# Optimization experiments

Measured on AMD Instinct MI355X. Metric: run time of the kernel, lower is better.

The kernel has to match this reference:

```python
import jax, jax.numpy as jnp
import numpy as np
from jax import lax

# --- static config (matches init_kwargs) ---
K_NAT, P_NAT, NHEAD, DM, L = 5, 2, 8, 128, 3
PK, OV, STRIDE = 4, 2, 2          # patcher kernel / overlap / stride = PK-OV
PPAD = PK - OV                    # circular pad for patcher/depatcher crop
RK, RC = 5, 12                    # res layer kernel, hidden channels = 3*4
DN = ('NCHW', 'OIHW', 'NCHW')


def setup_inputs() -> dict:
    key = jax.random.key(0)
    ks = jax.random.split(key, 16)
    B, C, H, W = 2, 3, 256, 256
    rn = lambda k, shape, s=0.02: jax.random.normal(k, shape, jnp.float32) * s
    return {
        'x': jax.random.normal(ks[0], (B, C, H, W), jnp.float32),
        'pos_w': jax.random.uniform(ks[1], (C, H, W), jnp.float32) + 0.5,
        'pos_b': jax.random.uniform(ks[2], (C, H, W), jnp.float32) - 0.5,
        'patch_w': rn(ks[3], (DM, C, PK, PK), 0.05),
        'patch_b': jnp.zeros((DM,), jnp.float32),
        'ln1_g': jnp.ones((L, DM), jnp.float32),
        'ln1_b': jnp.zeros((L, DM), jnp.float32),
        'qkv_w': rn(ks[4], (L, 3 * DM, DM)),
        'qkv_b': jnp.zeros((L, 3 * DM), jnp.float32),
        'rpb': rn(ks[5], (L, NHEAD, 2 * K_NAT - 1, 2 * K_NAT - 1)),
        'proj_w': rn(ks[6], (L, DM, DM)),
        'proj_b': jnp.zeros((L, DM), jnp.float32),
        'ln2_g': jnp.ones((L, DM), jnp.float32),
        'ln2_b': jnp.zeros((L, DM), jnp.float32),
        'fc1_w': rn(ks[7], (L, 4 * DM, DM)),
        'fc1_b': jnp.zeros((L, 4 * DM), jnp.float32),
        'fc2_w': rn(ks[8], (L, DM, 4 * DM)),
        'fc2_b': jnp.zeros((L, DM), jnp.float32),
        'depatch_w': rn(ks[9], (DM, C, PK, PK), 0.05),   # ConvTranspose2d weight (Cin,Cout,kh,kw)
        'depatch_b': jnp.zeros((C,), jnp.float32),
        'res_cv1_w': rn(ks[10], (RC, C, RK, RK), 0.05),
        'res_cv1_b': jnp.zeros((RC,), jnp.float32),
        'res_cv2_w': rn(ks[11], (C, RC, 1, 1), 0.05),
        'res_cv2_b': jnp.zeros((C,), jnp.float32),
    }


def _layer_norm(x, g, b):
    m = x.mean(-1, keepdims=True)
    v = x.var(-1, keepdims=True)
    return (x - m) * lax.rsqrt(v + 1e-5) * g + b


def _nat_block(x, ln1_g, ln1_b, qkv_w, qkv_b, rpb, proj_w, proj_b,
               ln2_g, ln2_b, fc1_w, fc1_b, fc2_w, fc2_b):
    # x: (B,H,W,C). NATLayer: LN -> circular pad by k//2 -> NA -> crop -> residual -> LN -> MLP -> residual.
    # After padding, every kept (interior) pixel has a full centered kxk neighborhood,
    # so we compute q only at interior positions and gather kxk K/V windows from the padded map.
    B, H, W, C = x.shape
    k, p, h = K_NAT, P_NAT, NHEAD
    dh = C // h
    y = _layer_norm(x, ln1_g, ln1_b)
    y = jnp.pad(y, ((0, 0), (p, p), (p, p), (0, 0)), mode='wrap')  # circular
    qkv = y @ qkv_w.T + qkv_b                                      # (B,H+2p,W+2p,3C)
    q, kk, vv = jnp.split(qkv, 3, axis=-1)
    q = q[:, p:p + H, p:p + W].reshape(B, H, W, h, dh) * (dh ** -0.5)
    def win(t):
        t = t.reshape(B, H + 2 * p, W + 2 * p, h, dh)
        return jnp.stack([t[:, i:i + H, j:j + W]
                          for i in range(k) for j in range(k)], axis=3)  # (B,H,W,k*k,h,dh)
    kw, vw = win(kk), win(vv)
    bias = rpb[:, p:p + k, p:p + k].reshape(h, k * k)  # centered slice of (2k-1,2k-1) RPB
    logits = jnp.einsum('bxyhd,bxynhd->bxyhn', q, kw) + bias
    a = jax.nn.softmax(logits, axis=-1)
    o = jnp.einsum('bxyhn,bxynhd->bxyhd', a, vw).reshape(B, H, W, C)
    x = x + (o @ proj_w.T + proj_b)
    y = _layer_norm(x, ln2_g, ln2_b)
    y = jax.nn.leaky_relu(y @ fc1_w.T + fc1_b) @ fc2_w.T + fc2_b
    return x + y


def _forward(x, pos_w, pos_b, patch_w, patch_b, ln1_g, ln1_b, qkv_w, qkv_b,
             rpb, proj_w, proj_b, ln2_g, ln2_b, fc1_w, fc1_b, fc2_w, fc2_b,
             depatch_w, depatch_b, res_cv1_w, res_cv1_b, res_cv2_w, res_cv2_b):
    # positional embedding (dropout is identity, p=0)
    x = x * pos_w + pos_b
    # OverlapConvPatcher: circular pad by (PK-OV), conv kernel PK stride PK-OV -> (B,129,129,DM)
    xp = jnp.pad(x, ((0, 0), (0, 0), (PPAD, PPAD), (PPAD, PPAD)), mode='wrap')
    f = lax.conv_general_dilated(xp, patch_w, (STRIDE, STRIDE), 'VALID',
                                 dimension_numbers=DN) + patch_b[None, :, None, None]
    f = f.transpose(0, 2, 3, 1)
    for i in range(L):
        f = _nat_block(f, ln1_g[i], ln1_b[i], qkv_w[i], qkv_b[i], rpb[i],
                       proj_w[i], proj_b[i], ln2_g[i], ln2_b[i],
                       fc1_w[i], fc1_b[i], fc2_w[i], fc2_b[i])
    # OverlapDeconvDepatcher: ConvTranspose2d (kernel PK, stride PK-OV), crop PPAD border
    f = f.transpose(0, 3, 1, 2)
    wf = jnp.flip(depatch_w, (2, 3)).transpose(1, 0, 2, 3)  # (Cout,Cin,kh,kw)
    y = lax.conv_general_dilated(f, wf, (1, 1), [(PK - 1, PK - 1)] * 2,
                                 lhs_dilation=(STRIDE, STRIDE),
                                 dimension_numbers=DN) + depatch_b[None, :, None, None]
    y = y[:, :, PPAD:-PPAD, PPAD:-PPAD]  # (B,3,256,256)
    # ResLayer: circular-pad same conv 5x5 -> leaky_relu -> 1x1 conv -> residual
    yp = jnp.pad(y, ((0, 0), (0, 0), (RK // 2, RK // 2), (RK // 2, RK // 2)), mode='wrap')
    r = lax.conv_general_dilated(yp, res_cv1_w, (1, 1), 'VALID',
                                 dimension_numbers=DN) + res_cv1_b[None, :, None, None]
    r = jax.nn.leaky_relu(r)
    r = lax.conv_general_dilated(r, res_cv2_w, (1, 1), 'VALID',
                                 dimension_numbers=DN) + res_cv2_b[None, :, None, None]
    return y + r


def reference(x, pos_w, pos_b, patch_w, patch_b, ln1_g, ln1_b, qkv_w, qkv_b,
              rpb, proj_w, proj_b, ln2_g, ln2_b, fc1_w, fc1_b, fc2_w, fc2_b,
              depatch_w, depatch_b, res_cv1_w, res_cv1_b, res_cv2_w, res_cv2_b):
    return _forward(x, pos_w, pos_b, patch_w, patch_b, ln1_g, ln1_b, qkv_w, qkv_b,
                    rpb, proj_w, proj_b, ln2_g, ln2_b, fc1_w, fc1_b, fc2_w, fc2_b,
                    depatch_w, depatch_b, res_cv1_w, res_cv1_b, res_cv2_w, res_cv2_b)
```

## Files before the change

### kernel.cpp

```cpp
#include <hip/hip_runtime.h>
#include <hip/hip_bf16.h>
#include <math.h>

#define HF 129
#define WF 129
#define BDIM 2
#define TOK (BDIM*HF*WF)
#define DMOD 128

typedef __attribute__((ext_vector_type(8))) short short8;
typedef __attribute__((ext_vector_type(8))) unsigned short ushort8;
typedef __attribute__((ext_vector_type(4))) float f32x4;

__device__ __forceinline__ float leaky(float v){ return v > 0.f ? v : 0.01f*v; }
__device__ __forceinline__ float bf2f(unsigned short u){ return __uint_as_float(((unsigned int)u) << 16); }
__device__ __forceinline__ unsigned short f2bf(float f){
    unsigned int u = __float_as_uint(f);
    unsigned int r = (u + 0x7fff + ((u >> 16) & 1)) >> 16;
    return (unsigned short)r;
}

#define NQ 147456
#define NPJ 49152
#define N1 196608
#define N2 196608
#define NPAT 8192
#define NDEP 8192
__global__ __launch_bounds__(256) void prep_weights(
    const float* __restrict__ qkv_w, const float* __restrict__ proj_w,
    const float* __restrict__ fc1_w, const float* __restrict__ fc2_w,
    const float* __restrict__ patch_w, const float* __restrict__ dep_w,
    __hip_bfloat16* __restrict__ wq, __hip_bfloat16* __restrict__ wp,
    __hip_bfloat16* __restrict__ w1, __hip_bfloat16* __restrict__ w2,
    __hip_bfloat16* __restrict__ wpat, __hip_bfloat16* __restrict__ wdep,
    float* __restrict__ zero64)
{
    int off = blockIdx.x*256 + threadIdx.x;
    if (off < NQ) { wq[off] = __float2bfloat16(qkv_w[off]); return; } off -= NQ;
    if (off < NPJ){ wp[off] = __float2bfloat16(proj_w[off]); return; } off -= NPJ;
    if (off < N1) { w1[off] = __float2bfloat16(fc1_w[off]); return; } off -= N1;
    if (off < N2) { w2[off] = __float2bfloat16(fc2_w[off]); return; } off -= N2;
    if (off < NPAT){ int r = off>>6, e = off&63;
        wpat[off] = __float2bfloat16(e < 48 ? patch_w[r*48 + e] : 0.f); return; } off -= NPAT;
    if (off < NDEP){ int e = off>>7, d = off&127;
        wdep[off] = __float2bfloat16(e < 48 ? dep_w[d*48 + e] : 0.f); return; } off -= NDEP;
    if (off < 64) zero64[off] = 0.f;
}

__global__ __launch_bounds__(256) void im2col_kernel(
    const float* __restrict__ x, const float* __restrict__ pos_w, const float* __restrict__ pos_b,
    __hip_bfloat16* __restrict__ G)
{
    __shared__ float xs[12][260];
    int blk = blockIdx.x;
    int b = blk / HF, oh = blk - b*HF;
    int tid = threadIdx.x;
    #pragma unroll
    for (int it = 0; it < 3; ++it) {
        int p = it*4 + (tid >> 6);
        int c = p >> 2, r = p & 3;
        int h = (oh*2 + r - 2 + 256) & 255;
        int w4 = (tid & 63) * 4;
        float4 xv  = *(const float4*)(x     + ((size_t)(b*3 + c)*256 + h)*256 + w4);
        float4 pwv = *(const float4*)(pos_w + ((size_t)c*256 + h)*256 + w4);
        float4 pbv = *(const float4*)(pos_b + ((size_t)c*256 + h)*256 + w4);
        float4 o; o.x = xv.x*pwv.x + pbv.x; o.y = xv.y*pwv.y + pbv.y;
        o.z = xv.z*pwv.z + pbv.z; o.w = xv.w*pwv.w + pbv.w;
        *(float4*)&xs[p][w4] = o;
    }
    __syncthreads();
    int e = tid & 63, og = tid >> 6;
    int c = e >> 4, k = e & 15, kh = k >> 2, kw = k & 3;
    int p = c*4 + kh;
    unsigned short* Grow = (unsigned short*)G + (size_t)blk*WF*64;
    for (int ow = og; ow < WF; ow += 4) {
        unsigned short v = 0;
        if (e < 48) {
            int col = (ow*2 + kw - 2 + 256) & 255;
            v = f2bf(xs[p][col]);
        }
        Grow[ow*64 + e] = v;
    }
}

template<int ACT, int RES, int OUTF, int LNE>
__global__ __launch_bounds__(256) void gemmF_kernel(
    const __hip_bfloat16* __restrict__ A, const __hip_bfloat16* __restrict__ W,
    const float* __restrict__ bias, const float* __restrict__ lng, const float* __restrict__ lnb,
    __hip_bfloat16* __restrict__ Cbf, float* __restrict__ Cf,
    __hip_bfloat16* __restrict__ yl, int M, int N, int K)
{
    __shared__ __align__(16) char As[64*128];
    __shared__ __align__(16) char Ws[128*128];
    __shared__ float2 lnred[64][2];
    int tid = threadIdx.x;
    int bm = blockIdx.x*64, bn = blockIdx.y*128;
    int lane = tid & 63, wid = tid >> 6;
    int wr = (wid >> 1)*32, wc = (wid & 1)*64;
    int lrow = lane & 15, lq = lane >> 4;
    int srow = tid >> 3, scg = tid & 7;
    int swz = (lrow & 7) << 4;
    int awo0 = ((srow     )*128 + scg*16) ^ ((srow&7)<<4);
    int awo1 = ((srow + 32)*128 + scg*16) ^ ((srow&7)<<4);

    bool v0 = (bm + srow) < M, v1 = (bm + srow + 32) < M;
    const __hip_bfloat16* a0p = A + (size_t)(bm + srow)*K + scg*8;
    const __hip_bfloat16* a1p = A + (size_t)(bm + srow + 32)*K + scg*8;
    const __hip_bfloat16* wp0 = W + (size_t)(bn + srow)*K + scg*8;

    f32x4 acc[2][4] = {};
    for (int k0 = 0; k0 < K; k0 += 64) {
        int4 va0 = {}, va1 = {};
        if (v0) va0 = *(const int4*)(a0p + k0);
        if (v1) va1 = *(const int4*)(a1p + k0);
        int4 vw0 = *(const int4*)(wp0 + k0);
        int4 vw1 = *(const int4*)(wp0 + (size_t)32*K + k0);
        int4 vw2 = *(const int4*)(wp0 + (size_t)64*K + k0);
        int4 vw3 = *(const int4*)(wp0 + (size_t)96*K + k0);
        __syncthreads();
        *(int4*)(As + awo0) = va0;
        *(int4*)(As + awo1) = va1;
        *(int4*)(Ws + awo0) = vw0;
        *(int4*)(Ws + awo1) = vw1;
        *(int4*)(Ws + (((srow+64)*128 + scg*16) ^ ((srow&7)<<4))) = vw2;
        *(int4*)(Ws + (((srow+96)*128 + scg*16) ^ ((srow&7)<<4))) = vw3;
        __syncthreads();
        #pragma unroll
        for (int ks = 0; ks < 2; ++ks) {
            int kb = ks*64;
            short8 af[2], bf[4];
            #pragma unroll
            for (int mi = 0; mi < 2; ++mi)
                af[mi] = *(const short8*)(As + (((wr + mi*16 + lrow)*128 + kb + lq*16) ^ swz));
            #pragma unroll
            for (int ni = 0; ni < 4; ++ni)
                bf[ni] = *(const short8*)(Ws + (((wc + ni*16 + lrow)*128 + kb + lq*16) ^ swz));
            #pragma unroll
            for (int mi = 0; mi < 2; ++mi)
                #pragma unroll
                for (int ni = 0; ni < 4; ++ni)
                    acc[mi][ni] = __builtin_amdgcn_mfma_f32_16x16x32_bf16(af[mi], bf[ni], acc[mi][ni], 0, 0, 0);
        }
    }
    float bcol[4];
    #pragma unroll
    for (int ni = 0; ni < 4; ++ni) bcol[ni] = bias[bn + wc + ni*16 + lrow];
    #pragma unroll
    for (int mi = 0; mi < 2; ++mi) {
        #pragma unroll
        for (int r = 0; r < 4; ++r) {
            int row = bm + wr + mi*16 + lq*4 + r;
            bool vrow = row < M;
            #pragma unroll
            for (int ni = 0; ni < 4; ++ni) {
                float v = acc[mi][ni][r] + bcol[ni];
                if (ACT) v = leaky(v);
                if (RES || OUTF) {
                    int col = wc + ni*16 + lrow;
                    size_t idx = (size_t)row*128 + col;
                    if (RES) { float old = vrow ? Cf[idx] : 0.f; v += old; }
                    if (vrow) Cf[idx] = v;
                } else {
                    int col = bn + wc + ni*16 + lrow;
                    if (vrow) Cbf[(size_t)row*N + col] = __float2bfloat16(v);
                }
                acc[mi][ni][r] = v;
            }
        }
    }
    if (LNE) {
        float sa[8], ssa[8];
        #pragma unroll
        for (int mi = 0; mi < 2; ++mi)
            #pragma unroll
            for (int r = 0; r < 4; ++r) {
                float s = 0.f, ss = 0.f;
                #pragma unroll
                for (int ni = 0; ni < 4; ++ni) { float v = acc[mi][ni][r]; s += v; ss += v*v; }
                sa[mi*4+r] = s; ssa[mi*4+r] = ss;
            }
        #pragma unroll
        for (int m = 1; m < 16; m <<= 1) {
            #pragma unroll
            for (int i = 0; i < 8; ++i) { sa[i] += __shfl_xor(sa[i], m); ssa[i] += __shfl_xor(ssa[i], m); }
        }
        if (lrow == 0) {
            #pragma unroll
            for (int i = 0; i < 8; ++i)
                lnred[wr + (i>>2)*16 + lq*4 + (i&3)][wc>>6] = make_float2(sa[i], ssa[i]);
        }
        __syncthreads();
        float gcol[4], bbcol[4];
        #pragma unroll
        for (int ni = 0; ni < 4; ++ni) {
            gcol[ni] = lng[wc + ni*16 + lrow];
            bbcol[ni] = lnb[wc + ni*16 + lrow];
        }
        #pragma unroll
        for (int mi = 0; mi < 2; ++mi) {
            #pragma unroll
            for (int r = 0; r < 4; ++r) {
                int rl = wr + mi*16 + lq*4 + r;
                int row = bm + rl;
                if (row >= M) continue;
                float2 h0 = lnred[rl][0], h1 = lnred[rl][1];
                float mean = (h0.x + h1.x) * (1.f/128.f);
                float var = (h0.y + h1.y) * (1.f/128.f) - mean*mean;
                float inv = rsqrtf(var + 1e-5f);
                #pragma unroll
                for (int ni = 0; ni < 4; ++ni) {
                    int col = wc + ni*16 + lrow;
                    float yv = (acc[mi][ni][r] - mean)*inv*gcol[ni] + bbcol[ni];
                    yl[(size_t)row*128 + col] = __float2bfloat16(yv);
                }
            }
        }
    }
}

template<int ACT, int RES, int OUTF, int A32>
__global__ __launch_bounds__(256) void mgemm_kernel(
    const void* __restrict__ Av, const __hip_bfloat16* __restrict__ W,
    const float* __restrict__ bias, __hip_bfloat16* __restrict__ Cbf,
    float* __restrict__ Cres, int M, int N, int K)
{
    __shared__ __align__(16) char As[64*128];
    __shared__ __align__(16) char Ws[64*128];
    int tid = threadIdx.x;
    int bm = blockIdx.x*64, bn = blockIdx.y*64;
    int lane = tid & 63, wid = tid >> 6;
    int wm = (wid >> 1)*32, wn = (wid & 1)*32;
    int lrow = lane & 15, lq = lane >> 4;
    int srow = tid >> 3, scg = tid & 7;
    int wo0 = ((srow     )*128 + scg*16) ^ ((srow&7)<<4);
    int wo1 = ((srow + 32)*128 + scg*16) ^ ((srow&7)<<4);
    int swz = (lrow & 7) << 4;
    int baseA0 = (wm + lrow     )*128 + lq*16;
    int baseA1 = (wm + 16 + lrow)*128 + lq*16;
    int baseB0 = (wn + lrow     )*128 + lq*16;
    int baseB1 = (wn + 16 + lrow)*128 + lq*16;

    f32x4 acc[2][2] = {};
    bool v0 = (bm + srow) < M, v1 = (bm + srow + 32) < M;
    const __hip_bfloat16* a0p = (const __hip_bfloat16*)Av + (size_t)(bm + srow)*K + scg*8;
    const __hip_bfloat16* a1p = (const __hip_bfloat16*)Av + (size_t)(bm + srow + 32)*K + scg*8;
    const float* a0pf = (const float*)Av + (size_t)(bm + srow)*K + scg*8;
    const float* a1pf = (const float*)Av + (size_t)(bm + srow + 32)*K + scg*8;
    const __hip_bfloat16* w0p = W + (size_t)(bn + srow)*K + scg*8;
    const __hip_bfloat16* w1p = W + (size_t)(bn + srow + 32)*K + scg*8;

    for (int k0 = 0; k0 < K; k0 += 64) {
        int4 va0 = {}, va1 = {};
        if (A32) {
            if (v0) {
                float4 p0 = *(const float4*)(a0pf + k0);
                float4 p1 = *(const float4*)(a0pf + k0 + 4);
                va0.x = f2bf(p0.x) | (f2bf(p0.y) << 16); va0.y = f2bf(p0.z) | (f2bf(p0.w) << 16);
                va0.z = f2bf(p1.x) | (f2bf(p1.y) << 16); va0.w = f2bf(p1.z) | (f2bf(p1.w) << 16);
            }
            if (v1) {
                float4 p0 = *(const float4*)(a1pf + k0);
                float4 p1 = *(const float4*)(a1pf + k0 + 4);
                va1.x = f2bf(p0.x) | (f2bf(p0.y) << 16); va1.y = f2bf(p0.z) | (f2bf(p0.w) << 16);
                va1.z = f2bf(p1.x) | (f2bf(p1.y) << 16); va1.w = f2bf(p1.z) | (f2bf(p1.w) << 16);
            }
        } else {
            if (v0) va0 = *(const int4*)(a0p + k0);
            if (v1) va1 = *(const int4*)(a1p + k0);
        }
        int4 vw0 = *(const int4*)(w0p + k0);
        int4 vw1 = *(const int4*)(w1p + k0);
        __syncthreads();
        *(int4*)(As + wo0) = va0;
        *(int4*)(As + wo1) = va1;
        *(int4*)(Ws + wo0) = vw0;
        *(int4*)(Ws + wo1) = vw1;
        __syncthreads();
        #pragma unroll
        for (int ks = 0; ks < 2; ++ks) {
            int kb = ks*64;
            short8 a0 = *(const short8*)(As + ((baseA0 + kb) ^ swz));
            short8 a1 = *(const short8*)(As + ((baseA1 + kb) ^ swz));
            short8 b0 = *(const short8*)(Ws + ((baseB0 + kb) ^ swz));
            short8 b1 = *(const short8*)(Ws + ((baseB1 + kb) ^ swz));
            acc[0][0] = __builtin_amdgcn_mfma_f32_16x16x32_bf16(a0, b0, acc[0][0], 0, 0, 0);
            acc[0][1] = __builtin_amdgcn_mfma_f32_16x16x32_bf16(a0, b1, acc[0][1], 0, 0, 0);
            acc[1][0] = __builtin_amdgcn_mfma_f32_16x16x32_bf16(a1, b0, acc[1][0], 0, 0, 0);
            acc[1][1] = __builtin_amdgcn_mfma_f32_16x16x32_bf16(a1, b1, acc[1][1], 0, 0, 0);
        }
    }
    float bv0 = bias[bn + wn + lrow];
    float bv1 = bias[bn + wn + 16 + lrow];
    #pragma unroll
    for (int mi = 0; mi < 2; ++mi) {
        #pragma unroll
        for (int r = 0; r < 4; ++r) {
            int row = bm + wm + mi*16 + lq*4 + r;
            if (row >= M) continue;
            #pragma unroll
            for (int ni = 0; ni < 2; ++ni) {
                float v = acc[mi][ni][r] + (ni ? bv1 : bv0);
                if (ACT == 1) v = leaky(v);
                int col = bn + wn + ni*16 + lrow;
                if (RES)       Cres[(size_t)row*N + col] += v;
                else if (OUTF) Cres[(size_t)row*N + col] = v;
                else           Cbf[(size_t)row*N + col] = __float2bfloat16(v);
            }
        }
    }
}

__global__ __launch_bounds__(256) void attn_kernel(const __hip_bfloat16* __restrict__ qkv,
    const float* __restrict__ rpb, __hip_bfloat16* __restrict__ o)
{
    int gid = blockIdx.x*256 + threadIdx.x;
    int tok = gid >> 3;
    if (tok >= TOK) return;
    int head = gid & 7;
    int b = tok / (HF*WF);
    int rem = tok - b*HF*WF;
    int y = rem / WF, x = rem - y*WF;
    const ushort8* qp = (const ushort8*)(qkv + (size_t)tok*384 + head*16);
    float q[16];
    {
        ushort8 u0 = qp[0], u1 = qp[1];
        #pragma unroll
        for (int i = 0; i < 8; ++i) { q[i] = bf2f(u0[i])*0.25f; q[i+8] = bf2f(u1[i])*0.25f; }
    }
    float logits[25];
    float mx = -1e30f;
    #pragma unroll
    for (int di = -2; di <= 2; ++di) {
        int ny = y + di; ny += (ny < 0) ? HF : 0; ny -= (ny >= HF) ? HF : 0;
        #pragma unroll
        for (int dj = -2; dj <= 2; ++dj) {
            int nx = x + dj; nx += (nx < 0) ? WF : 0; nx -= (nx >= WF) ? WF : 0;
            size_t nt = (size_t)((b*HF + ny)*WF + nx);
            const ushort8* kp = (const ushort8*)(qkv + nt*384 + 128 + head*16);
            ushort8 k0 = kp[0], k1 = kp[1];
            float d = 0.f;
            #pragma unroll
            for (int i = 0; i < 8; ++i) d += q[i]*bf2f(k0[i]) + q[i+8]*bf2f(k1[i]);
            d += rpb[head*81 + (di+4)*9 + (dj+4)];
            logits[(di+2)*5 + (dj+2)] = d;
            mx = fmaxf(mx, d);
        }
    }
    float s = 0.f;
    #pragma unroll
    for (int n = 0; n < 25; ++n) { float p = __expf(logits[n]-mx); logits[n] = p; s += p; }
    float invs = 1.f/s;
    float outv[16] = {};
    #pragma unroll
    for (int di = -2; di <= 2; ++di) {
        int ny = y + di; ny += (ny < 0) ? HF : 0; ny -= (ny >= HF) ? HF : 0;
        #pragma unroll
        for (int dj = -2; dj <= 2; ++dj) {
            int nx = x + dj; nx += (nx < 0) ? WF : 0; nx -= (nx >= WF) ? WF : 0;
            size_t nt = (size_t)((b*HF + ny)*WF + nx);
            const ushort8* vp = (const ushort8*)(qkv + nt*384 + 256 + head*16);
            ushort8 v0 = vp[0], v1 = vp[1];
            float p = logits[(di+2)*5 + (dj+2)];
            #pragma unroll
            for (int i = 0; i < 8; ++i) { outv[i] += p*bf2f(v0[i]); outv[i+8] += p*bf2f(v1[i]); }
        }
    }
    __hip_bfloat16* op = o + (size_t)tok*DMOD + head*16;
    #pragma unroll
    for (int i = 0; i < 16; ++i) op[i] = __float2bfloat16(outv[i]*invs);
}

__global__ __launch_bounds__(256) void degather_kernel(const float* __restrict__ G,
    const float* __restrict__ db, float* __restrict__ yimg)
{
    int idx = blockIdx.x*256 + threadIdx.x;
    int b = idx >> 16;
    int pix = idx & 65535;
    int i = pix >> 8, j = pix & 255;
    int fh0 = i >> 1, fw0 = j >> 1;
    size_t r00 = ((size_t)(b*HF + fh0)*WF + fw0)*64;
    size_t r01 = r00 + 64;
    size_t r10 = r00 + (size_t)WF*64;
    size_t r11 = r10 + 64;
    int wr0 = (2 + (i & 1))*4, wr1 = (i & 1)*4;
    int wc0 = 2 + (j & 1), wc1 = (j & 1);
    #pragma unroll
    for (int c = 0; c < 3; ++c) {
        int e = c*16;
        float v = db[c]
                + G[r00 + e + wr0 + wc0] + G[r01 + e + wr0 + wc1]
                + G[r10 + e + wr1 + wc0] + G[r11 + e + wr1 + wc1];
        yimg[((size_t)(b*3 + c) << 16) + pix] = v;
    }
}

__global__ __launch_bounds__(256) void res_kernel(const float* __restrict__ y,
    const float* __restrict__ w1, const float* __restrict__ b1,
    const float* __restrict__ w2, const float* __restrict__ b2, float* __restrict__ out)
{
    int idx = blockIdx.x*256 + threadIdx.x;
    int b = idx >> 16;
    int pix = idx & 65535;
    int i = pix >> 8, j = pix & 255;
    float yv[3][5][5];
    #pragma unroll
    for (int c = 0; c < 3; ++c) {
        #pragma unroll
        for (int u = 0; u < 5; ++u) {
            int ii = (i + u - 2 + 256) & 255;
            #pragma unroll
            for (int v = 0; v < 5; ++v) {
                int jj = (j + v - 2 + 256) & 255;
                yv[c][u][v] = y[((size_t)(b*3 + c)*256 + ii)*256 + jj];
            }
        }
    }
    float r1[12];
    #pragma unroll
    for (int rc = 0; rc < 12; ++rc) {
        float a = b1[rc];
        #pragma unroll
        for (int c = 0; c < 3; ++c)
            #pragma unroll
            for (int u = 0; u < 5; ++u)
                #pragma unroll
                for (int v = 0; v < 5; ++v)
                    a += yv[c][u][v] * w1[rc*75 + c*25 + u*5 + v];
        r1[rc] = leaky(a);
    }
    #pragma unroll
    for (int c = 0; c < 3; ++c) {
        float a = b2[c];
        #pragma unroll
        for (int rc = 0; rc < 12; ++rc) a += r1[rc]*w2[c*12 + rc];
        out[((size_t)(b*3 + c)*256 + i)*256 + j] = yv[c][2][2] + a;
    }
}

extern "C" void kernel_launch(void* const* d_in, const int* in_sizes, int n_in,
                              void* d_out, int out_size, void* d_ws, size_t ws_size,
                              hipStream_t stream)
{
    const float* x      = (const float*)d_in[0];
    const float* pos_w  = (const float*)d_in[1];
    const float* pos_b  = (const float*)d_in[2];
    const float* patch_w= (const float*)d_in[3];
    const float* patch_b= (const float*)d_in[4];
    const float* ln1_g  = (const float*)d_in[5];
    const float* ln1_b  = (const float*)d_in[6];
    const float* qkv_w  = (const float*)d_in[7];
    const float* qkv_b  = (const float*)d_in[8];
    const float* rpb    = (const float*)d_in[9];
    const float* proj_w = (const float*)d_in[10];
    const float* proj_b = (const float*)d_in[11];
    const float* ln2_g  = (const float*)d_in[12];
    const float* ln2_b  = (const float*)d_in[13];
    const float* fc1_w  = (const float*)d_in[14];
    const float* fc1_b  = (const float*)d_in[15];
    const float* fc2_w  = (const float*)d_in[16];
    const float* fc2_b  = (const float*)d_in[17];
    const float* dep_w  = (const float*)d_in[18];
    const float* dep_b  = (const float*)d_in[19];
    const float* rc1_w  = (const float*)d_in[20];
    const float* rc1_b  = (const float*)d_in[21];
    const float* rc2_w  = (const float*)d_in[22];
    const float* rc2_b  = (const float*)d_in[23];

    const size_t SZ = (size_t)TOK * 128;
    char* w = (char*)d_ws;
    float* f            = (float*)w;            w += SZ*4;
    __hip_bfloat16* yln = (__hip_bfloat16*)w;   w += SZ*2;
    __hip_bfloat16* ao  = (__hip_bfloat16*)w;   w += SZ*2;
    __hip_bfloat16* qkvb= (__hip_bfloat16*)w;   w += (size_t)TOK*384*2;
    __hip_bfloat16* hb  = (__hip_bfloat16*)w;   w += (size_t)TOK*512*2;
    float* yimg         = (float*)w;            w += (size_t)BDIM*3*65536*4;
    __hip_bfloat16* wq  = (__hip_bfloat16*)w;   w += (size_t)NQ*2;
    __hip_bfloat16* wp  = (__hip_bfloat16*)w;   w += (size_t)NPJ*2;
    __hip_bfloat16* w1  = (__hip_bfloat16*)w;   w += (size_t)N1*2;
    __hip_bfloat16* w2  = (__hip_bfloat16*)w;   w += (size_t)N2*2;
    __hip_bfloat16* wpat= (__hip_bfloat16*)w;   w += (size_t)NPAT*2;
    __hip_bfloat16* wdep= (__hip_bfloat16*)w;   w += (size_t)NDEP*2;
    float* zero64       = (float*)w;            w += 64*4;

    __hip_bfloat16* icol = qkvb;
    float* G             = (float*)hb;

    const int PREP_TOT = NQ + NPJ + N1 + N2 + NPAT + NDEP + 64;
    prep_weights<<<(PREP_TOT + 255)/256, 256, 0, stream>>>(
        qkv_w, proj_w, fc1_w, fc2_w, patch_w, dep_w, wq, wp, w1, w2, wpat, wdep, zero64);

    im2col_kernel<<<BDIM*HF, 256, 0, stream>>>(x, pos_w, pos_b, icol);

    const int GM = (TOK + 63)/64;

    gemmF_kernel<0,0,1,1><<<dim3(GM,1), 256, 0, stream>>>(icol, wpat, patch_b,
        ln1_g, ln1_b, nullptr, f, yln, TOK, 128, 64);

    for (int l = 0; l < 3; ++l) {
        gemmF_kernel<0,0,0,0><<<dim3(GM,3), 256, 0, stream>>>(yln, wq + (size_t)l*384*128,
            qkv_b + l*384, nullptr, nullptr, qkvb, nullptr, nullptr, TOK, 384, 128);
        attn_kernel<<<(TOK*8 + 255)/256, 256, 0, stream>>>(qkvb, rpb + l*8*81, ao);
        gemmF_kernel<0,1,0,1><<<dim3(GM,1), 256, 0, stream>>>(ao, wp + (size_t)l*128*128,
            proj_b + l*128, ln2_g + l*128, ln2_b + l*128, nullptr, f, yln, TOK, 128, 128);
        gemmF_kernel<1,0,0,0><<<dim3(GM,4), 256, 0, stream>>>(yln, w1 + (size_t)l*512*128,
            fc1_b + l*512, nullptr, nullptr, hb, nullptr, nullptr, TOK, 512, 128);
        if (l < 2)
            gemmF_kernel<0,1,0,1><<<dim3(GM,1), 256, 0, stream>>>(hb, w2 + (size_t)l*128*512,
                fc2_b + l*128, ln1_g + (l+1)*128, ln1_b + (l+1)*128, nullptr, f, yln, TOK, 128, 512);
        else
            gemmF_kernel<0,1,0,0><<<dim3(GM,1), 256, 0, stream>>>(hb, w2 + (size_t)l*128*512,
                fc2_b + l*128, nullptr, nullptr, nullptr, f, nullptr, TOK, 128, 512);
    }

    mgemm_kernel<0,0,1,1><<<dim3(GM,1), 256, 0, stream>>>(f, wdep, zero64,
        nullptr, G, TOK, 64, 128);
    degather_kernel<<<512, 256, 0, stream>>>(G, dep_b, yimg);

    res_kernel<<<512, 256, 0, stream>>>(yimg, rc1_w, rc1_b, rc2_w, rc2_b, (float*)d_out);
}
```

Measured before the change: 361.3 us.

## Tile neighborhood attention with shared-memory K/V halo per 8x8 block

Replaces the per-token neighborhood attention kernel with a tiled version. Each block stages the K and V rows for a 12x12 halo window around an 8x8 token tile into swizzled LDS, so the 25 neighbor reads come from shared memory rather than repeated global loads. Outputs are packed into 16-byte stores instead of scalar bf16 stores. In exchange it uses 72KB of LDS per block, which caps occupancy, and edge tiles (129 is not a multiple of 8) do redundant work.

```diff
diff --git a/kernel.cpp b/kernel.cpp
--- a/kernel.cpp
+++ b/kernel.cpp
@@ -14,10 +14,9 @@
 
 __device__ __forceinline__ float leaky(float v){ return v > 0.f ? v : 0.01f*v; }
 __device__ __forceinline__ float bf2f(unsigned short u){ return __uint_as_float(((unsigned int)u) << 16); }
-__device__ __forceinline__ unsigned short f2bf(float f){
+__device__ __forceinline__ unsigned int f2bf(float f){
     unsigned int u = __float_as_uint(f);
-    unsigned int r = (u + 0x7fff + ((u >> 16) & 1)) >> 16;
-    return (unsigned short)r;
+    return (u + 0x7fff + ((u >> 16) & 1)) >> 16;
 }
 
 #define NQ 147456
@@ -77,7 +76,7 @@
         unsigned short v = 0;
         if (e < 48) {
             int col = (ow*2 + kw - 2 + 256) & 255;
-            v = f2bf(xs[p][col]);
+            v = (unsigned short)f2bf(xs[p][col]);
         }
         Grow[ow*64 + e] = v;
     }
@@ -218,6 +217,104 @@
     }
 }
 
+__global__ __launch_bounds__(256) void attn_tile_kernel(
+    const __hip_bfloat16* __restrict__ qkv, const float* __restrict__ rpb,
+    __hip_bfloat16* __restrict__ o)
+{
+    __shared__ __align__(16) char Kl[144*256];
+    __shared__ __align__(16) char Vl[144*256];
+    int blk = blockIdx.x;
+    int b = blk / 289;
+    int rem = blk - b*289;
+    int tyi = rem / 17, txi = rem - tyi*17;
+    int y0 = tyi*8, x0 = txi*8;
+    int tid = threadIdx.x;
+
+    #pragma unroll
+    for (int it = 0; it < 18; ++it) {
+        int u = tid + it*256;
+        int wtok = u >> 5;
+        int half = (u >> 4) & 1;
+        int c = u & 15;
+        int wy = wtok / 12, wx = wtok - wy*12;
+        int gy = y0 + wy - 2; gy += (gy < 0) ? HF : 0; gy -= (gy >= HF) ? HF : 0;
+        int gx = x0 + wx - 2; gx += (gx < 0) ? WF : 0; gx -= (gx >= WF) ? WF : 0;
+        size_t tok = (size_t)(b*HF + gy)*WF + gx;
+        int4 v = *(const int4*)(qkv + tok*384 + 128 + half*128 + c*8);
+        char* dst = half ? Vl : Kl;
+        *(int4*)(dst + wtok*256 + ((c*16) ^ ((wtok & 7) << 4))) = v;
+    }
+    __syncthreads();
+
+    #pragma unroll
+    for (int pp = 0; pp < 2; ++pp) {
+        int pr = tid + pp*256;
+        int tloc = pr >> 3;
+        int head = pr & 7;
+        int ty = tloc >> 3, tx = tloc & 7;
+        int gy = y0 + ty, gx = x0 + tx;
+        bool valid = (gy < HF) && (gx < WF);
+        int cy = valid ? gy : HF-1, cx = valid ? gx : WF-1;
+        size_t tok = (size_t)(b*HF + cy)*WF + cx;
+        const ushort8* qp = (const ushort8*)(qkv + tok*384 + head*16);
+        float q[16];
+        {
+            ushort8 u0 = qp[0], u1 = qp[1];
+            #pragma unroll
+            for (int i = 0; i < 8; ++i) { q[i] = bf2f(u0[i])*0.25f; q[i+8] = bf2f(u1[i])*0.25f; }
+        }
+        const float* rb = rpb + head*81;
+        float logits[25];
+        float mx = -1e30f;
+        #pragma unroll
+        for (int di = 0; di < 5; ++di) {
+            #pragma unroll
+            for (int dj = 0; dj < 5; ++dj) {
+                int wtok = (ty + di)*12 + tx + dj;
+                int sw = (wtok & 7) << 4;
+                ushort8 k0 = *(const ushort8*)(Kl + wtok*256 + ((head*32) ^ sw));
+                ushort8 k1 = *(const ushort8*)(Kl + wtok*256 + ((head*32 + 16) ^ sw));
+                float d = 0.f;
+                #pragma unroll
+                for (int i = 0; i < 8; ++i) d += q[i]*bf2f(k0[i]) + q[i+8]*bf2f(k1[i]);
+                d += rb[(di+2)*9 + dj + 2];
+                logits[di*5 + dj] = d;
+                mx = fmaxf(mx, d);
+            }
+        }
+        float s = 0.f;
+        #pragma unroll
+        for (int n = 0; n < 25; ++n) { float p = __expf(logits[n]-mx); logits[n] = p; s += p; }
+        float invs = 1.f/s;
+        float outv[16] = {};
+        #pragma unroll
+        for (int di = 0; di < 5; ++di) {
+            #pragma unroll
+            for (int dj = 0; dj < 5; ++dj) {
+                int wtok = (ty + di)*12 + tx + dj;
+                int sw = (wtok & 7) << 4;
+                ushort8 v0 = *(const ushort8*)(Vl + wtok*256 + ((head*32) ^ sw));
+                ushort8 v1 = *(const ushort8*)(Vl + wtok*256 + ((head*32 + 16) ^ sw));
+                float p = logits[di*5 + dj];
+                #pragma unroll
+                for (int i = 0; i < 8; ++i) { outv[i] += p*bf2f(v0[i]); outv[i+8] += p*bf2f(v1[i]); }
+            }
+        }
+        if (valid) {
+            int4 w0, w1;
+            unsigned int pk[8];
+            #pragma unroll
+            for (int i = 0; i < 8; ++i)
+                pk[i] = f2bf(outv[2*i]*invs) | (f2bf(outv[2*i+1]*invs) << 16);
+            w0.x = (int)pk[0]; w0.y = (int)pk[1]; w0.z = (int)pk[2]; w0.w = (int)pk[3];
+            w1.x = (int)pk[4]; w1.y = (int)pk[5]; w1.z = (int)pk[6]; w1.w = (int)pk[7];
+            __hip_bfloat16* op = o + tok*128 + head*16;
+            *(int4*)op = w0;
+            *(int4*)(op + 8) = w1;
+        }
+    }
+}
+
 template<int ACT, int RES, int OUTF, int A32>
 __global__ __launch_bounds__(256) void mgemm_kernel(
     const void* __restrict__ Av, const __hip_bfloat16* __restrict__ W,
@@ -255,14 +352,14 @@
             if (v0) {
                 float4 p0 = *(const float4*)(a0pf + k0);
                 float4 p1 = *(const float4*)(a0pf + k0 + 4);
-                va0.x = f2bf(p0.x) | (f2bf(p0.y) << 16); va0.y = f2bf(p0.z) | (f2bf(p0.w) << 16);
-                va0.z = f2bf(p1.x) | (f2bf(p1.y) << 16); va0.w = f2bf(p1.z) | (f2bf(p1.w) << 16);
+                va0.x = (int)(f2bf(p0.x) | (f2bf(p0.y) << 16)); va0.y = (int)(f2bf(p0.z) | (f2bf(p0.w) << 16));
+                va0.z = (int)(f2bf(p1.x) | (f2bf(p1.y) << 16)); va0.w = (int)(f2bf(p1.z) | (f2bf(p1.w) << 16));
             }
             if (v1) {
                 float4 p0 = *(const float4*)(a1pf + k0);
                 float4 p1 = *(const float4*)(a1pf + k0 + 4);
-                va1.x = f2bf(p0.x) | (f2bf(p0.y) << 16); va1.y = f2bf(p0.z) | (f2bf(p0.w) << 16);
-                va1.z = f2bf(p1.x) | (f2bf(p1.y) << 16); va1.w = f2bf(p1.z) | (f2bf(p1.w) << 16);
+                va1.x = (int)(f2bf(p0.x) | (f2bf(p0.y) << 16)); va1.y = (int)(f2bf(p0.z) | (f2bf(p0.w) << 16));
+                va1.z = (int)(f2bf(p1.x) | (f2bf(p1.y) << 16)); va1.w = (int)(f2bf(p1.z) | (f2bf(p1.w) << 16));
             }
         } else {
             if (v0) va0 = *(const int4*)(a0p + k0);
@@ -308,66 +405,6 @@
             }
         }
     }
-}
-
-__global__ __launch_bounds__(256) void attn_kernel(const __hip_bfloat16* __restrict__ qkv,
-    const float* __restrict__ rpb, __hip_bfloat16* __restrict__ o)
-{
-    int gid = blockIdx.x*256 + threadIdx.x;
-    int tok = gid >> 3;
-    if (tok >= TOK) return;
-    int head = gid & 7;
-    int b = tok / (HF*WF);
-    int rem = tok - b*HF*WF;
-    int y = rem / WF, x = rem - y*WF;
-    const ushort8* qp = (const ushort8*)(qkv + (size_t)tok*384 + head*16);
-    float q[16];
-    {
-        ushort8 u0 = qp[0], u1 = qp[1];
-        #pragma unroll
-        for (int i = 0; i < 8; ++i) { q[i] = bf2f(u0[i])*0.25f; q[i+8] = bf2f(u1[i])*0.25f; }
-    }
-    float logits[25];
-    float mx = -1e30f;
-    #pragma unroll
-    for (int di = -2; di <= 2; ++di) {
-        int ny = y + di; ny += (ny < 0) ? HF : 0; ny -= (ny >= HF) ? HF : 0;
-        #pragma unroll
-        for (int dj = -2; dj <= 2; ++dj) {
-            int nx = x + dj; nx += (nx < 0) ? WF : 0; nx -= (nx >= WF) ? WF : 0;
-            size_t nt = (size_t)((b*HF + ny)*WF + nx);
-            const ushort8* kp = (const ushort8*)(qkv + nt*384 + 128 + head*16);
-            ushort8 k0 = kp[0], k1 = kp[1];
-            float d = 0.f;
-            #pragma unroll
-            for (int i = 0; i < 8; ++i) d += q[i]*bf2f(k0[i]) + q[i+8]*bf2f(k1[i]);
-            d += rpb[head*81 + (di+4)*9 + (dj+4)];
-            logits[(di+2)*5 + (dj+2)] = d;
-            mx = fmaxf(mx, d);
-        }
-    }
-    float s = 0.f;
-    #pragma unroll
-    for (int n = 0; n < 25; ++n) { float p = __expf(logits[n]-mx); logits[n] = p; s += p; }
-    float invs = 1.f/s;
-    float outv[16] = {};
-    #pragma unroll
-    for (int di = -2; di <= 2; ++di) {
-        int ny = y + di; ny += (ny < 0) ? HF : 0; ny -= (ny >= HF) ? HF : 0;
-        #pragma unroll
-        for (int dj = -2; dj <= 2; ++dj) {
-            int nx = x + dj; nx += (nx < 0) ? WF : 0; nx -= (nx >= WF) ? WF : 0;
-            size_t nt = (size_t)((b*HF + ny)*WF + nx);
-            const ushort8* vp = (const ushort8*)(qkv + nt*384 + 256 + head*16);
-            ushort8 v0 = vp[0], v1 = vp[1];
-            float p = logits[(di+2)*5 + (dj+2)];
-            #pragma unroll
-            for (int i = 0; i < 8; ++i) { outv[i] += p*bf2f(v0[i]); outv[i+8] += p*bf2f(v1[i]); }
-        }
-    }
-    __hip_bfloat16* op = o + (size_t)tok*DMOD + head*16;
-    #pragma unroll
-    for (int i = 0; i < 16; ++i) op[i] = __float2bfloat16(outv[i]*invs);
 }
 
 __global__ __launch_bounds__(256) void degather_kernel(const float* __restrict__ G,
@@ -492,6 +529,7 @@
     im2col_kernel<<<BDIM*HF, 256, 0, stream>>>(x, pos_w, pos_b, icol);
 
     const int GM = (TOK + 63)/64;
+    const int NTILE = 17*17*BDIM;
 
     gemmF_kernel<0,0,1,1><<<dim3(GM,1), 256, 0, stream>>>(icol, wpat, patch_b,
         ln1_g, ln1_b, nullptr, f, yln, TOK, 128, 64);
@@ -499,7 +537,7 @@
     for (int l = 0; l < 3; ++l) {
         gemmF_kernel<0,0,0,0><<<dim3(GM,3), 256, 0, stream>>>(yln, wq + (size_t)l*384*128,
             qkv_b + l*384, nullptr, nullptr, qkvb, nullptr, nullptr, TOK, 384, 128);
-        attn_kernel<<<(TOK*8 + 255)/256, 256, 0, stream>>>(qkvb, rpb + l*8*81, ao);
+        attn_tile_kernel<<<NTILE, 256, 0, stream>>>(qkvb, rpb + l*8*81, ao);
         gemmF_kernel<0,1,0,1><<<dim3(GM,1), 256, 0, stream>>>(ao, wp + (size_t)l*128*128,
             proj_b + l*128, ln2_g + l*128, ln2_b + l*128, nullptr, f, yln, TOK, 128, 128);
         gemmF_kernel<1,0,0,0><<<dim3(GM,4), 256, 0, stream>>>(yln, w1 + (size_t)l*512*128,
```

Result: slower. 387.6 us (+7.3%).
